# Performance work log

Hardware: AMD Instinct MI355X
Metric: run time of the kernel (lower is better)

## Reference

```python
import jax, jax.numpy as jnp
import numpy as np

DIM_IN, DIM, BS, H, W = 128, 64, 32, 64, 64
G, K = 5, 3          # KAN grid intervals and spline degree
EPS = 1e-5           # BatchNorm eps


def conv2d(x, w, b, groups=1, pad=0):
    # x: [B,C,H,W], w: [O, C//groups, kh, kw]
    y = jax.lax.conv_general_dilated(
        x, w, window_strides=(1, 1), padding=[(pad, pad), (pad, pad)],
        dimension_numbers=('NCHW', 'OIHW', 'NCHW'), feature_group_count=groups)
    return y + b[None, :, None, None]


def bn(x, g, b, m, v):
    # inference-mode BatchNorm2d
    inv = jax.lax.rsqrt(v + EPS)
    return g[None, :, None, None] * (x - m[None, :, None, None]) * inv[None, :, None, None] + b[None, :, None, None]


def make_grid():
    # extended knot vector over [-1,1], G intervals, degree K: G+2K+1 knots
    h = 2.0 / G
    t = jnp.arange(-K, G + K + 1, dtype=jnp.float32) * h - 1.0
    return jnp.broadcast_to(t, (DIM, G + 2 * K + 1))


def bspline_basis(x, t, k):
    # Cox-de Boor recursion. x: [N,in], t: [in, G+2k+1] -> B: [N,in,G+k]
    xe = x[..., None]
    B = ((xe >= t[:, :-1]) & (xe < t[:, 1:])).astype(x.dtype)
    for p in range(1, k + 1):
        B = ((xe - t[:, :-(p + 1)]) / (t[:, p:-1] - t[:, :-(p + 1)])) * B[..., :-1] \
          + ((t[:, p + 1:] - xe) / (t[:, p + 1:] - t[:, 1:-p])) * B[..., 1:]
    return B


def kan_forward(xk, coef, scale_base, scale_sp, kan_bias):
    # single KANLayer [dim -> dim]: silu residual branch + spline branch + node bias
    t = make_grid()
    B = bspline_basis(xk, t, K)                      # [N, in, G+K]
    y_base = jax.nn.silu(xk) @ scale_base            # [N, out]
    y_sp = jnp.einsum('nij,ioj->no', B, coef * scale_sp[:, :, None])
    return y_base + y_sp + kan_bias


def setup_inputs() -> dict:
    key = jax.random.key(0)
    ks = jax.random.split(key, 24)
    rn = lambda k, s, sc=0.05: jax.random.normal(k, s, jnp.float32) * sc
    return {
        'x': jax.random.normal(ks[0], (BS, DIM_IN, H, W), jnp.float32),
        'reduce_w': rn(ks[1], (DIM, DIM_IN, 1, 1), 0.1), 'reduce_b': rn(ks[2], (DIM,)),
        'dw_w': rn(ks[3], (DIM, 1, 7, 7), 0.1), 'dw_b': rn(ks[4], (DIM,)),
        'dw_g': 1.0 + rn(ks[5], (DIM,)), 'dw_beta': rn(ks[6], (DIM,)),
        'dw_m': rn(ks[7], (DIM,)), 'dw_v': 0.5 + jax.random.uniform(ks[8], (DIM,)),
        'f2_w': rn(ks[9], (DIM, DIM, 1, 1), 0.1), 'f2_b': rn(ks[10], (DIM,)),
        'coef': rn(ks[11], (DIM, DIM, G + K), 0.1),
        'scale_base': 1.0 / np.sqrt(DIM) + rn(ks[12], (DIM, DIM)),
        'scale_sp': 1.0 + rn(ks[13], (DIM, DIM)),
        'kan_bias': rn(ks[14], (DIM,)),
        'g_w': rn(ks[15], (DIM, DIM, 1, 1), 0.1), 'g_b': rn(ks[16], (DIM,)),
        'g_g': 1.0 + rn(ks[17], (DIM,)), 'g_beta': rn(ks[18], (DIM,)),
        'g_m': rn(ks[19], (DIM,)), 'g_v': 0.5 + jax.random.uniform(ks[20], (DIM,)),
        'dw2_w': rn(ks[21], (DIM, 1, 7, 7), 0.1), 'dw2_b': rn(ks[22], (DIM,)),
    }


def reference(x, reduce_w, reduce_b, dw_w, dw_b, dw_g, dw_beta, dw_m, dw_v,
              f2_w, f2_b, coef, scale_base, scale_sp, kan_bias,
              g_w, g_b, g_g, g_beta, g_m, g_v, dw2_w, dw2_b):
    x = conv2d(x, reduce_w, reduce_b)                       # dim_reduce 1x1
    inp = x
    xd = bn(conv2d(x, dw_w, dw_b, groups=DIM, pad=3), dw_g, dw_beta, dw_m, dw_v)  # 7x7 dwconv + BN
    bs, dim, h, w = xd.shape
    xk = xd.transpose(0, 2, 3, 1).reshape(bs * h * w, dim)  # tokenwise view
    x1 = kan_forward(xk, coef, scale_base, scale_sp, kan_bias)
    x1 = x1.reshape(bs, h, w, dim).transpose(0, 3, 1, 2)    # back to NCHW
    x2 = conv2d(xd, f2_w, f2_b)                             # f2 1x1
    y = x1 * x2                                             # elementwise gate
    y = bn(conv2d(y, g_w, g_b), g_g, g_beta, g_m, g_v)      # g 1x1 + BN
    y = conv2d(y, dw2_w, dw2_b, groups=DIM, pad=3)          # dwconv2 7x7
    return inp + y
```

## Files before the change

kernel.cpp:

```cpp
#include <hip/hip_runtime.h>
#include <hip/hip_bf16.h>

#define BSZ 32
#define CIN 128
#define CD 64
#define HH 64
#define WW 64
#define PLANE (HH * WW)
#define NPIX (BSZ * HH * WW)
#define NB 8
#define BN_EPS 1e-5f

typedef __attribute__((ext_vector_type(8))) short short8v;
typedef __attribute__((ext_vector_type(4))) float f32x4;
typedef __attribute__((ext_vector_type(4))) unsigned int u32x4;

static __device__ __forceinline__ short f2bf(float f) {
    __hip_bfloat16 h = __float2bfloat16(f);
    return __builtin_bit_cast(short, h);
}
static __device__ __forceinline__ unsigned int cvtpk(float lo, float hi) {
    unsigned int r;
    asm("v_cvt_pk_bf16_f32 %0, %1, %2" : "=v"(r) : "v"(lo), "v"(hi));
    return r;
}

__global__ __launch_bounds__(256) void k_prep(
    const float* __restrict__ coef, const float* __restrict__ ssp,
    const float* __restrict__ sb, const float* __restrict__ f2w,
    const float* __restrict__ reduce_w, const float* __restrict__ g_w,
    const float* __restrict__ dw_g, const float* __restrict__ dw_beta,
    const float* __restrict__ dw_m, const float* __restrict__ dw_v,
    const float* __restrict__ dw_b, const float* __restrict__ g_g,
    const float* __restrict__ g_beta, const float* __restrict__ g_m,
    const float* __restrict__ g_v, const float* __restrict__ g_b,
    short* __restrict__ W1f, short* __restrict__ W2f,
    short* __restrict__ WRf, short* __restrict__ WGf,
    float* __restrict__ cbuf)
{
    const int idx = blockIdx.x * 256 + threadIdx.x;
    if (idx < 36864) {
        const int e = idx & 7, l = (idx >> 3) & 63, c = (idx >> 9) & 3, s = idx >> 11;
        const int k = s * 32 + ((l >> 4) << 3) + e;
        const int j = (c << 4) + (l & 15);
        float v;
        if (k < 512) {
            const int i = k >> 3, t = k & 7;
            v = coef[(i * 64 + j) * 8 + t] * ssp[i * 64 + j];
        } else {
            v = sb[(k - 512) * 64 + j];
        }
        W1f[idx] = f2bf(v);
    } else if (idx < 45056) {
        const int f = idx - 36864;
        const int e = f & 7, l = (f >> 3) & 63, c = (f >> 9) & 3, s = f >> 11;
        const int k = s * 32 + ((l >> 4) << 3) + e;
        const int j = (c << 4) + (l & 15);
        W2f[f] = f2bf(f2w[j * 64 + k]);
    } else if (idx < 53248) {
        const int f = idx - 45056;
        const int e = f & 7, l = (f >> 3) & 63, c = (f >> 9) & 3, s = f >> 11;
        const int k = s * 32 + ((l >> 4) << 3) + e;
        const int j = (c << 4) + (l & 15);
        WRf[f] = f2bf(reduce_w[j * CIN + k]);
    } else if (idx < 57344) {
        const int f = idx - 53248;
        const int e = f & 7, l = (f >> 3) & 63, c = (f >> 9) & 3, s = f >> 11;
        const int k = s * 32 + ((l >> 4) << 3) + e;
        const int j = (c << 4) + (l & 15);
        WGf[f] = f2bf(g_w[j * 64 + k]);
    } else if (idx < 57600) {
        const int q = (idx - 57344) >> 6, c = idx & 63;
        if (q == 0) cbuf[c] = dw_g[c] * rsqrtf(dw_v[c] + BN_EPS);
        else if (q == 1) {
            float sc = dw_g[c] * rsqrtf(dw_v[c] + BN_EPS);
            cbuf[64 + c] = (dw_b[c] - dw_m[c]) * sc + dw_beta[c];
        } else if (q == 2) cbuf[128 + c] = g_g[c] * rsqrtf(g_v[c] + BN_EPS);
// ... 75 lines not shown
    float K[49];
#pragma unroll
    for (int q = 0; q < 49; ++q) K[q] = wp[q];
    const float scl = RESID ? 1.f : sc[c];
    const float shf = shv[c];
    const float* rplane = RESID ? (resid + pbase) : nullptr;
    float* oplane = out + pbase;

    float acc[7] = {0.f, 0.f, 0.f, 0.f, 0.f, 0.f, 0.f};
#pragma unroll
    for (int rr = 0; rr < 22; ++rr) {
        const int ra = H0 + rr - 3;
        float rowv = 0.f;
        if (ra >= 0 && ra < 64) rowv = plane[ra * 64 + lane];
        float sh[7];
        sh[3] = rowv;
#pragma unroll
        for (int d = 1; d <= 3; ++d) {
            float tp = __shfl(rowv, lane + d);
            sh[3 + d] = (lane + d < 64) ? tp : 0.f;
            float tm = __shfl(rowv, lane - d);
            sh[3 - d] = (lane - d >= 0) ? tm : 0.f;
        }
#pragma unroll
        for (int dy = 0; dy < 7; ++dy) {
            const int o = rr - dy;
            if (o >= 0 && o < 16) {
                const int slot = o % 7;
#pragma unroll
                for (int dx = 0; dx < 7; ++dx)
                    acc[slot] = fmaf(sh[dx], K[dy * 7 + dx], acc[slot]);
            }
        }
        const int done = rr - 6;
        if (done >= 0 && done < 16) {
            const int slot = done % 7;
            const int h = H0 + done;
            float val;
            if (RESID) val = acc[slot] + shf + rplane[h * 64 + lane];
            else       val = acc[slot] * scl + shf;
            oplane[h * 64 + lane] = val;
            acc[slot] = 0.f;
        }
    }
}

__global__ __launch_bounds__(256) void k_kan_fused(
    const float* __restrict__ xd, const short* __restrict__ W1f,
    const short* __restrict__ W2f, const short* __restrict__ WGf,
    const float* __restrict__ kb, const float* __restrict__ f2b,
    const float* __restrict__ gs, const float* __restrict__ gsh,
    float* __restrict__ z)
{
    __shared__ __align__(16) short As1[2 * 18 * 64 * 8];
    __shared__ __align__(16) short As2[2 * 2 * 64 * 8];
    const int tid = threadIdx.x;
    const int tg0 = blockIdx.x * 32;
    const int bb = tg0 >> 12, pix0 = tg0 & 4095;
    const float* xb = xd + (size_t)bb * CD * PLANE + pix0;
    const int tkn = tid & 31;
    const int w5 = tid >> 5;
    const int mt = tkn >> 4, m = tkn & 15;

    float vf[8], sf[8];
#pragma unroll
    for (int p = 0; p < 8; ++p) {
        const int c = w5 * 8 + p;
        const float v = xb[(size_t)c * PLANE + tkn];
        vf[p] = v;
        sf[p] = v * __builtin_amdgcn_rcpf(1.0f + __expf(-v));

        const float tt = (v + 2.2f) * 2.5f;
        const float fi = floorf(tt);
        const int i0 = (int)fi;
        const float u = tt - fi;
        const bool inr = (tt >= 0.0f) && (tt < 11.0f);
        const float u2 = u * u, u3 = u2 * u;
        const float t1 = 1.f - u;
        const float w0 = (1.f / 6.f) * t1 * t1 * t1;
        const float w3 = (1.f / 6.f) * u3;
        const float w1 = fmaf(0.5f, u3, 2.f / 3.f) - u2;
        const float w2 = 1.f - w0 - w1 - w3;
        const unsigned W01 = cvtpk(w0, w1);
        const unsigned W23 = cvtpk(w2, w3);
        const int q0 = i0 - 3;
        int a = q0 >> 1;
        const int bpar = q0 & 1;
        if (!inr) a = 100;
        const unsigned A1c = (W01 >> 16) | (W23 << 16);
        const unsigned C0 = bpar ? (W01 << 16) : W01;
        const unsigned C1 = bpar ? A1c : W23;
        const unsigned C2 = bpar ? (W23 >> 16) : 0u;
        u32x4 D;
        D.x = (a == 0) ? C0 : (a == -1) ? C1 : (a == -2) ? C2 : 0u;
        D.y = (a == 1) ? C0 : (a == 0) ? C1 : (a == -1) ? C2 : 0u;
        D.z = (a == 2) ? C0 : (a == 1) ? C1 : (a == 0) ? C2 : 0u;
        D.w = (a == 3) ? C0 : (a == 2) ? C1 : (a == 1) ? C2 : 0u;

        const int s = w5 * 2 + (p >> 2);
        const int phys = (((p & 3) << 4) | m) ^ (s & 7);
        *(u32x4*)&As1[((mt * 18 + s) * 64 + phys) * 8] = D;
    }
    {
        short8v vpk, spk;
#pragma unroll
        for (int q = 0; q < 4; ++q) {
            ((unsigned*)&vpk)[q] = cvtpk(vf[2 * q], vf[2 * q + 1]);
            ((unsigned*)&spk)[q] = cvtpk(sf[2 * q], sf[2 * q + 1]);
        }
        const int slot = ((w5 & 3) << 4) | m;
        const int s2 = 16 + (w5 >> 2);
        *(short8v*)&As1[((mt * 18 + s2) * 64 + (slot ^ (s2 & 7))) * 8] = spk;
        const int s3 = w5 >> 2;
        *(short8v*)&As2[((mt * 2 + s3) * 64 + (slot ^ (s3 & 7))) * 8] = vpk;
    }
    __syncthreads();

    const int cw = tid >> 6, l = tid & 63;
    f32x4 accA0 = {0.f,0.f,0.f,0.f}, accA1 = {0.f,0.f,0.f,0.f};
    f32x4 accB0 = {0.f,0.f,0.f,0.f}, accB1 = {0.f,0.f,0.f,0.f};
#pragma unroll 1
    for (int s = 0; s < 18; ++s) {
        const short8v bfr = *(const short8v*)&W1f[((s * 4 + cw) * 64 + l) * 8];
        const short8v a0 = *(const short8v*)&As1[((0 * 18 + s) * 64 + (l ^ (s & 7))) * 8];
        const short8v a1 = *(const short8v*)&As1[((1 * 18 + s) * 64 + (l ^ (s & 7))) * 8];
        accA0 = __builtin_amdgcn_mfma_f32_16x16x32_bf16(a0, bfr, accA0, 0, 0, 0);
        accA1 = __builtin_amdgcn_mfma_f32_16x16x32_bf16(a1, bfr, accA1, 0, 0, 0);
    }
#pragma unroll
    for (int s = 0; s < 2; ++s) {
        const short8v bfr = *(const short8v*)&W2f[((s * 4 + cw) * 64 + l) * 8];
        const short8v a0 = *(const short8v*)&As2[((0 * 2 + s) * 64 + (l ^ s)) * 8];
        const short8v a1 = *(const short8v*)&As2[((1 * 2 + s) * 64 + (l ^ s)) * 8];
        accB0 = __builtin_amdgcn_mfma_f32_16x16x32_bf16(a0, bfr, accB0, 0, 0, 0);
        accB1 = __builtin_amdgcn_mfma_f32_16x16x32_bf16(a1, bfr, accB1, 0, 0, 0);
    }

    const int j = (cw << 4) + (l & 15);
    const float kbj = kb[j], f2bj = f2b[j];
    const int rb = (l >> 4) << 2;
    float y0[4], y1[4];
#pragma unroll
    for (int r = 0; r < 4; ++r) {
        y0[r] = (accA0[r] + kbj) * (accB0[r] + f2bj);
        y1[r] = (accA1[r] + kbj) * (accB1[r] + f2bj);
    }
    __syncthreads();

    float* Ysh = (float*)As1;
#pragma unroll
    for (int r = 0; r < 4; ++r) {
        Ysh[j * 33 + rb + r]      = y0[r];
        Ysh[j * 33 + 16 + rb + r] = y1[r];
    }
    __syncthreads();

    {
        float yv[8];
#pragma unroll
        for (int p = 0; p < 8; ++p) yv[p] = Ysh[(w5 * 8 + p) * 33 + tkn];
        short8v ypk;
#pragma unroll
        for (int q = 0; q < 4; ++q)
            ((unsigned*)&ypk)[q] = cvtpk(yv[2 * q], yv[2 * q + 1]);
        const int slot = ((w5 & 3) << 4) | m;
        const int s3 = w5 >> 2;
        *(short8v*)&As2[((mt * 2 + s3) * 64 + (slot ^ (s3 & 7))) * 8] = ypk;
    }
    __syncthreads();

    f32x4 acc30 = {0.f,0.f,0.f,0.f}, acc31 = {0.f,0.f,0.f,0.f};
#pragma unroll
    for (int s = 0; s < 2; ++s) {
        const short8v bfr = *(const short8v*)&WGf[((s * 4 + cw) * 64 + l) * 8];
        const short8v a0 = *(const short8v*)&As2[((0 * 2 + s) * 64 + (l ^ s)) * 8];
        const short8v a1 = *(const short8v*)&As2[((1 * 2 + s) * 64 + (l ^ s)) * 8];
        acc30 = __builtin_amdgcn_mfma_f32_16x16x32_bf16(a0, bfr, acc30, 0, 0, 0);
        acc31 = __builtin_amdgcn_mfma_f32_16x16x32_bf16(a1, bfr, acc31, 0, 0, 0);
    }

    float* Osh = (float*)As1;
    const float sj = gs[j], hj = gsh[j];
#pragma unroll
    for (int r = 0; r < 4; ++r) {
        Osh[j * 33 + rb + r]      = acc30[r] * sj + hj;
        Osh[j * 33 + 16 + rb + r] = acc31[r] * sj + hj;
    }
    __syncthreads();
    float* zb = z + (size_t)bb * CD * PLANE + pix0;
#pragma unroll
    for (int q = 0; q < 8; ++q) {
        const int idx = tid + (q << 8);
        const int jj = idx >> 5, t2 = idx & 31;
        zb[(size_t)jj * PLANE + t2] = Osh[jj * 33 + t2];
    }
}

extern "C" void kernel_launch(void* const* d_in, const int* in_sizes, int n_in,
                              void* d_out, int out_size, void* d_ws, size_t ws_size,
                              hipStream_t stream)
{
    (void)in_sizes; (void)n_in; (void)out_size; (void)ws_size;
    const float* x        = (const float*)d_in[0];
    const float* reduce_w = (const float*)d_in[1];
    const float* reduce_b = (const float*)d_in[2];
    const float* dw_w     = (const float*)d_in[3];
    const float* dw_b     = (const float*)d_in[4];
    const float* dw_g     = (const float*)d_in[5];
    const float* dw_beta  = (const float*)d_in[6];
    const float* dw_m     = (const float*)d_in[7];
    const float* dw_v     = (const float*)d_in[8];
    const float* f2_w     = (const float*)d_in[9];
    const float* f2_b     = (const float*)d_in[10];
    const float* coef     = (const float*)d_in[11];
    const float* sbase    = (const float*)d_in[12];
    const float* ssp      = (const float*)d_in[13];
    const float* kbias    = (const float*)d_in[14];
    const float* g_w      = (const float*)d_in[15];
    const float* g_b      = (const float*)d_in[16];
    const float* g_g      = (const float*)d_in[17];
    const float* g_beta   = (const float*)d_in[18];
    const float* g_m      = (const float*)d_in[19];
    const float* g_v      = (const float*)d_in[20];
    const float* dw2_w    = (const float*)d_in[21];
    const float* dw2_b    = (const float*)d_in[22];
    float* out = (float*)d_out;

    const size_t NEL = (size_t)BSZ * CD * PLANE;
    short* W1f = (short*)d_ws;
    short* W2f = W1f + 36864;
    short* WRf = W2f + 8192;
    short* WGf = WRf + 8192;
    float* cbuf = (float*)((char*)d_ws + 115200);
    float* inp = (float*)((char*)d_ws + 131072);
    float* xdb = inp + NEL;
    float* z   = xdb + NEL;

    k_prep<<<225, 256, 0, stream>>>(coef, ssp, sbase, f2_w, reduce_w, g_w,
                                    dw_g, dw_beta, dw_m, dw_v, dw_b,
                                    g_g, g_beta, g_m, g_v, g_b,
                                    W1f, W2f, WRf, WGf, cbuf);
    k_reduce_mfma<<<BSZ * 32, 256, 0, stream>>>(x, WRf, reduce_b, inp);
    k_dwconv<false><<<BSZ * 16 * 4, 256, 0, stream>>>(inp, dw_w, cbuf, cbuf + 64, nullptr, xdb);
    k_kan_fused<<<NPIX / 32, 256, 0, stream>>>(xdb, W1f, W2f, WGf, kbias, f2_b,
                                               cbuf + 128, cbuf + 192, z);
    k_dwconv<true><<<BSZ * 16 * 4, 256, 0, stream>>>(z, dw2_w, nullptr, dw2_b, inp, out);
}
```

Baseline: 105.8 us.

## Process KAN fused tile as two 16-token passes to halve LDS use

The fused KAN/gate/g-conv kernel previously staged all 32 tokens per block in shared memory at once and kept two MFMA accumulator sets per wave. It now loops over two 16-token halves, reusing a half-size LDS buffer and a single accumulator set, with each thread computing 4 channels instead of 8. This cuts LDS footprint and register pressure to allow higher occupancy. The cost is extra barriers per block, weight fragments reloaded from global memory for each half, and 16-wide global stores that coalesce worse.

```diff
diff --git a/kernel.cpp b/kernel.cpp
--- a/kernel.cpp
+++ b/kernel.cpp
@@ -204,147 +204,135 @@
     const float* __restrict__ gs, const float* __restrict__ gsh,
     float* __restrict__ z)
 {
-    __shared__ __align__(16) short As1[2 * 18 * 64 * 8];
-    __shared__ __align__(16) short As2[2 * 2 * 64 * 8];
+    __shared__ __align__(16) short As1[18 * 64 * 8];
+    __shared__ __align__(16) short As2[2 * 64 * 8];
     const int tid = threadIdx.x;
     const int tg0 = blockIdx.x * 32;
     const int bb = tg0 >> 12, pix0 = tg0 & 4095;
     const float* xb = xd + (size_t)bb * CD * PLANE + pix0;
-    const int tkn = tid & 31;
-    const int w5 = tid >> 5;
-    const int mt = tkn >> 4, m = tkn & 15;
-
-    float vf[8], sf[8];
-#pragma unroll
-    for (int p = 0; p < 8; ++p) {
-        const int c = w5 * 8 + p;
-        const float v = xb[(size_t)c * PLANE + tkn];
-        vf[p] = v;
-        sf[p] = v * __builtin_amdgcn_rcpf(1.0f + __expf(-v));
-
-        const float tt = (v + 2.2f) * 2.5f;
-        const float fi = floorf(tt);
-        const int i0 = (int)fi;
-        const float u = tt - fi;
-        const bool inr = (tt >= 0.0f) && (tt < 11.0f);
-        const float u2 = u * u, u3 = u2 * u;
-        const float t1 = 1.f - u;
-        const float w0 = (1.f / 6.f) * t1 * t1 * t1;
-        const float w3 = (1.f / 6.f) * u3;
-        const float w1 = fmaf(0.5f, u3, 2.f / 3.f) - u2;
-        const float w2 = 1.f - w0 - w1 - w3;
-        const unsigned W01 = cvtpk(w0, w1);
-        const unsigned W23 = cvtpk(w2, w3);
-        const int q0 = i0 - 3;
-        int a = q0 >> 1;
-        const int bpar = q0 & 1;
-        if (!inr) a = 100;
-        const unsigned A1c = (W01 >> 16) | (W23 << 16);
-        const unsigned C0 = bpar ? (W01 << 16) : W01;
-        const unsigned C1 = bpar ? A1c : W23;
-        const unsigned C2 = bpar ? (W23 >> 16) : 0u;
-        u32x4 D;
-        D.x = (a == 0) ? C0 : (a == -1) ? C1 : (a == -2) ? C2 : 0u;
-        D.y = (a == 1) ? C0 : (a == 0) ? C1 : (a == -1) ? C2 : 0u;
-        D.z = (a == 2) ? C0 : (a == 1) ? C1 : (a == 0) ? C2 : 0u;
-        D.w = (a == 3) ? C0 : (a == 2) ? C1 : (a == 1) ? C2 : 0u;
-
-        const int s = w5 * 2 + (p >> 2);
-        const int phys = (((p & 3) << 4) | m) ^ (s & 7);
-        *(u32x4*)&As1[((mt * 18 + s) * 64 + phys) * 8] = D;
-    }
-    {
-        short8v vpk, spk;
+    float* zb = z + (size_t)bb * CD * PLANE + pix0;
+    const int tkn = tid & 15;
+    const int grp = tid >> 4;
+    const int m = tkn;
+    const int cw = tid >> 6, l = tid & 63;
+    const int j = (cw << 4) + (l & 15);
+    const int rb = (l >> 4) << 2;
+    const float kbj = kb[j], f2bj = f2b[j];
+    const float sj = gs[j], hj = gsh[j];
+    const int gfield = (grp >> 1) & 3;
+    const int slot16 = (gfield << 4) | m;
+    const int e0 = (grp & 1) * 4;
+
+#pragma unroll 1
+    for (int g = 0; g < 2; ++g) {
+        const int toff = g * 16;
+        float vf[4], sf[4];
+#pragma unroll
+        for (int p = 0; p < 4; ++p) {
+            const int c = grp * 4 + p;
+            const float v = xb[(size_t)c * PLANE + toff + tkn];
+            vf[p] = v;
+            sf[p] = v * __builtin_amdgcn_rcpf(1.0f + __expf(-v));
+
+            const float tt = (v + 2.2f) * 2.5f;
+            const float fi = floorf(tt);
+            const int i0 = (int)fi;
+            const float u = tt - fi;
+            const bool inr = (tt >= 0.0f) && (tt < 11.0f);
+            const float u2 = u * u, u3 = u2 * u;
+            const float t1 = 1.f - u;
+            const float w0 = (1.f / 6.f) * t1 * t1 * t1;
+            const float w3 = (1.f / 6.f) * u3;
+            const float w1 = fmaf(0.5f, u3, 2.f / 3.f) - u2;
+            const float w2 = 1.f - w0 - w1 - w3;
+            const unsigned W01 = cvtpk(w0, w1);
+            const unsigned W23 = cvtpk(w2, w3);
+            const int q0 = i0 - 3;
+            int a = q0 >> 1;
+            const int bpar = q0 & 1;
+            if (!inr) a = 100;
+            const unsigned A1c = (W01 >> 16) | (W23 << 16);
+            const unsigned C0 = bpar ? (W01 << 16) : W01;
+            const unsigned C1 = bpar ? A1c : W23;
+            const unsigned C2 = bpar ? (W23 >> 16) : 0u;
+            u32x4 D;
+            D.x = (a == 0) ? C0 : (a == -1) ? C1 : (a == -2) ? C2 : 0u;
+            D.y = (a == 1) ? C0 : (a == 0) ? C1 : (a == -1) ? C2 : 0u;
+            D.z = (a == 2) ? C0 : (a == 1) ? C1 : (a == 0) ? C2 : 0u;
+            D.w = (a == 3) ? C0 : (a == 2) ? C1 : (a == 1) ? C2 : 0u;
+
+            const int s = c >> 2;
+            const int phys = ((p << 4) | m) ^ (s & 7);
+            *(u32x4*)&As1[(s * 64 + phys) * 8] = D;
+        }
+        {
+            uint2 sv, vv;
+            sv.x = cvtpk(sf[0], sf[1]); sv.y = cvtpk(sf[2], sf[3]);
+            vv.x = cvtpk(vf[0], vf[1]); vv.y = cvtpk(vf[2], vf[3]);
+            const int s2 = 16 + (grp >> 3);
+            *(uint2*)&As1[(s2 * 64 + (slot16 ^ (s2 & 7))) * 8 + e0] = sv;
+            const int s3 = grp >> 3;
+            *(uint2*)&As2[(s3 * 64 + (slot16 ^ (s3 & 7))) * 8 + e0] = vv;
+        }
+        __syncthreads();
+
+        f32x4 accA = {0.f,0.f,0.f,0.f}, accB = {0.f,0.f,0.f,0.f};
+#pragma unroll 1
+        for (int s = 0; s < 18; ++s) {
+            const short8v bfr = *(const short8v*)&W1f[((s * 4 + cw) * 64 + l) * 8];
+            const short8v a0 = *(const short8v*)&As1[(s * 64 + (l ^ (s & 7))) * 8];
+            accA = __builtin_amdgcn_mfma_f32_16x16x32_bf16(a0, bfr, accA, 0, 0, 0);
+        }
+#pragma unroll
+        for (int s = 0; s < 2; ++s) {
+            const short8v bfr = *(const short8v*)&W2f[((s * 4 + cw) * 64 + l) * 8];
+            const short8v a0 = *(const short8v*)&As2[(s * 64 + (l ^ s)) * 8];
+            accB = __builtin_amdgcn_mfma_f32_16x16x32_bf16(a0, bfr, accB, 0, 0, 0);
+        }
+
+        float y0[4];
+#pragma unroll
+        for (int r = 0; r < 4; ++r)
+            y0[r] = (accA[r] + kbj) * (accB[r] + f2bj);
+        __syncthreads();
+
+        float* Ysh = (float*)As1;
+#pragma unroll
+        for (int r = 0; r < 4; ++r) Ysh[j * 17 + rb + r] = y0[r];
+        __syncthreads();
+
+        {
+            float yv[4];
+#pragma unroll
+            for (int p = 0; p < 4; ++p) yv[p] = Ysh[(grp * 4 + p) * 17 + tkn];
+            uint2 yy;
+            yy.x = cvtpk(yv[0], yv[1]); yy.y = cvtpk(yv[2], yv[3]);
+            const int s3 = grp >> 3;
+            *(uint2*)&As2[(s3 * 64 + (slot16 ^ (s3 & 7))) * 8 + e0] = yy;
+        }
+        __syncthreads();
+
+        f32x4 acc3 = {0.f,0.f,0.f,0.f};
+#pragma unroll
+        for (int s = 0; s < 2; ++s) {
+            const short8v bfr = *(const short8v*)&WGf[((s * 4 + cw) * 64 + l) * 8];
+            const short8v a0 = *(const short8v*)&As2[(s * 64 + (l ^ s)) * 8];
+            acc3 = __builtin_amdgcn_mfma_f32_16x16x32_bf16(a0, bfr, acc3, 0, 0, 0);
+        }
+
+        float* Osh = (float*)As1;
+#pragma unroll
+        for (int r = 0; r < 4; ++r)
+            Osh[j * 17 + rb + r] = acc3[r] * sj + hj;
+        __syncthreads();
+
 #pragma unroll
         for (int q = 0; q < 4; ++q) {
-            ((unsigned*)&vpk)[q] = cvtpk(vf[2 * q], vf[2 * q + 1]);
-            ((unsigned*)&spk)[q] = cvtpk(sf[2 * q], sf[2 * q + 1]);
-        }
-        const int slot = ((w5 & 3) << 4) | m;
-        const int s2 = 16 + (w5 >> 2);
-        *(short8v*)&As1[((mt * 18 + s2) * 64 + (slot ^ (s2 & 7))) * 8] = spk;
-        const int s3 = w5 >> 2;
-        *(short8v*)&As2[((mt * 2 + s3) * 64 + (slot ^ (s3 & 7))) * 8] = vpk;
-    }
-    __syncthreads();
-
-    const int cw = tid >> 6, l = tid & 63;
-    f32x4 accA0 = {0.f,0.f,0.f,0.f}, accA1 = {0.f,0.f,0.f,0.f};
-    f32x4 accB0 = {0.f,0.f,0.f,0.f}, accB1 = {0.f,0.f,0.f,0.f};
-#pragma unroll 1
-    for (int s = 0; s < 18; ++s) {
-        const short8v bfr = *(const short8v*)&W1f[((s * 4 + cw) * 64 + l) * 8];
-        const short8v a0 = *(const short8v*)&As1[((0 * 18 + s) * 64 + (l ^ (s & 7))) * 8];
-        const short8v a1 = *(const short8v*)&As1[((1 * 18 + s) * 64 + (l ^ (s & 7))) * 8];
-        accA0 = __builtin_amdgcn_mfma_f32_16x16x32_bf16(a0, bfr, accA0, 0, 0, 0);
-        accA1 = __builtin_amdgcn_mfma_f32_16x16x32_bf16(a1, bfr, accA1, 0, 0, 0);
-    }
-#pragma unroll
-    for (int s = 0; s < 2; ++s) {
-        const short8v bfr = *(const short8v*)&W2f[((s * 4 + cw) * 64 + l) * 8];
-        const short8v a0 = *(const short8v*)&As2[((0 * 2 + s) * 64 + (l ^ s)) * 8];
-        const short8v a1 = *(const short8v*)&As2[((1 * 2 + s) * 64 + (l ^ s)) * 8];
-        accB0 = __builtin_amdgcn_mfma_f32_16x16x32_bf16(a0, bfr, accB0, 0, 0, 0);
-        accB1 = __builtin_amdgcn_mfma_f32_16x16x32_bf16(a1, bfr, accB1, 0, 0, 0);
-    }
-
-    const int j = (cw << 4) + (l & 15);
-    const float kbj = kb[j], f2bj = f2b[j];
-    const int rb = (l >> 4) << 2;
-    float y0[4], y1[4];
-#pragma unroll
-    for (int r = 0; r < 4; ++r) {
-        y0[r] = (accA0[r] + kbj) * (accB0[r] + f2bj);
-        y1[r] = (accA1[r] + kbj) * (accB1[r] + f2bj);
-    }
-    __syncthreads();
-
-    float* Ysh = (float*)As1;
-#pragma unroll
-    for (int r = 0; r < 4; ++r) {
-        Ysh[j * 33 + rb + r]      = y0[r];
-        Ysh[j * 33 + 16 + rb + r] = y1[r];
-    }
-    __syncthreads();
-
-    {
-        float yv[8];
-#pragma unroll
-        for (int p = 0; p < 8; ++p) yv[p] = Ysh[(w5 * 8 + p) * 33 + tkn];
-        short8v ypk;
-#pragma unroll
-        for (int q = 0; q < 4; ++q)
-            ((unsigned*)&ypk)[q] = cvtpk(yv[2 * q], yv[2 * q + 1]);
-        const int slot = ((w5 & 3) << 4) | m;
-        const int s3 = w5 >> 2;
-        *(short8v*)&As2[((mt * 2 + s3) * 64 + (slot ^ (s3 & 7))) * 8] = ypk;
-    }
-    __syncthreads();
-
-    f32x4 acc30 = {0.f,0.f,0.f,0.f}, acc31 = {0.f,0.f,0.f,0.f};
-#pragma unroll
-    for (int s = 0; s < 2; ++s) {
-        const short8v bfr = *(const short8v*)&WGf[((s * 4 + cw) * 64 + l) * 8];
-        const short8v a0 = *(const short8v*)&As2[((0 * 2 + s) * 64 + (l ^ s)) * 8];
-        const short8v a1 = *(const short8v*)&As2[((1 * 2 + s) * 64 + (l ^ s)) * 8];
-        acc30 = __builtin_amdgcn_mfma_f32_16x16x32_bf16(a0, bfr, acc30, 0, 0, 0);
-        acc31 = __builtin_amdgcn_mfma_f32_16x16x32_bf16(a1, bfr, acc31, 0, 0, 0);
-    }
-
-    float* Osh = (float*)As1;
-    const float sj = gs[j], hj = gsh[j];
-#pragma unroll
-    for (int r = 0; r < 4; ++r) {
-        Osh[j * 33 + rb + r]      = acc30[r] * sj + hj;
-        Osh[j * 33 + 16 + rb + r] = acc31[r] * sj + hj;
-    }
-    __syncthreads();
-    float* zb = z + (size_t)bb * CD * PLANE + pix0;
-#pragma unroll
-    for (int q = 0; q < 8; ++q) {
-        const int idx = tid + (q << 8);
-        const int jj = idx >> 5, t2 = idx & 31;
-        zb[(size_t)jj * PLANE + t2] = Osh[jj * 33 + t2];
+            const int idx = tid + (q << 8);
+            const int jj = idx >> 4, t2 = idx & 15;
+            zb[(size_t)jj * PLANE + toff + t2] = Osh[jj * 17 + t2];
+        }
+        __syncthreads();
     }
 }
 
```

Measured after the change: 112.6 us. 6.4% more time.

## Process two token tiles per KAN block with register-resident weights and prefetch

Applied to the files above, without the earlier changes.

The fused KAN/gate kernel now handles 64 tokens per block in two 32-token iterations, half the blocks. The bf16 weight fragments (W1, W2, WG) are loaded into registers once per block instead of once per tile. The next tile's input is prefetched into registers while the current one is processed. This raises register pressure (about 88 VGPRs of weights), which may lower occupancy, and the tile loop adds one extra barrier per iteration.

```diff
diff --git a/kernel.cpp b/kernel.cpp
--- a/kernel.cpp
+++ b/kernel.cpp
@@ -207,144 +207,166 @@
     __shared__ __align__(16) short As1[2 * 18 * 64 * 8];
     __shared__ __align__(16) short As2[2 * 2 * 64 * 8];
     const int tid = threadIdx.x;
-    const int tg0 = blockIdx.x * 32;
+    const int tg0 = blockIdx.x * 64;
     const int bb = tg0 >> 12, pix0 = tg0 & 4095;
     const float* xb = xd + (size_t)bb * CD * PLANE + pix0;
+    float* zb = z + (size_t)bb * CD * PLANE + pix0;
     const int tkn = tid & 31;
     const int w5 = tid >> 5;
     const int mt = tkn >> 4, m = tkn & 15;
-
-    float vf[8], sf[8];
-#pragma unroll
-    for (int p = 0; p < 8; ++p) {
-        const int c = w5 * 8 + p;
-        const float v = xb[(size_t)c * PLANE + tkn];
-        vf[p] = v;
-        sf[p] = v * __builtin_amdgcn_rcpf(1.0f + __expf(-v));
-
-        const float tt = (v + 2.2f) * 2.5f;
-        const float fi = floorf(tt);
-        const int i0 = (int)fi;
-        const float u = tt - fi;
-        const bool inr = (tt >= 0.0f) && (tt < 11.0f);
-        const float u2 = u * u, u3 = u2 * u;
-        const float t1 = 1.f - u;
-        const float w0 = (1.f / 6.f) * t1 * t1 * t1;
-        const float w3 = (1.f / 6.f) * u3;
-        const float w1 = fmaf(0.5f, u3, 2.f / 3.f) - u2;
-        const float w2 = 1.f - w0 - w1 - w3;
-        const unsigned W01 = cvtpk(w0, w1);
-        const unsigned W23 = cvtpk(w2, w3);
-        const int q0 = i0 - 3;
-        int a = q0 >> 1;
-        const int bpar = q0 & 1;
-        if (!inr) a = 100;
-        const unsigned A1c = (W01 >> 16) | (W23 << 16);
-        const unsigned C0 = bpar ? (W01 << 16) : W01;
-        const unsigned C1 = bpar ? A1c : W23;
-        const unsigned C2 = bpar ? (W23 >> 16) : 0u;
-        u32x4 D;
-        D.x = (a == 0) ? C0 : (a == -1) ? C1 : (a == -2) ? C2 : 0u;
-        D.y = (a == 1) ? C0 : (a == 0) ? C1 : (a == -1) ? C2 : 0u;
-        D.z = (a == 2) ? C0 : (a == 1) ? C1 : (a == 0) ? C2 : 0u;
-        D.w = (a == 3) ? C0 : (a == 2) ? C1 : (a == 1) ? C2 : 0u;
-
-        const int s = w5 * 2 + (p >> 2);
-        const int phys = (((p & 3) << 4) | m) ^ (s & 7);
-        *(u32x4*)&As1[((mt * 18 + s) * 64 + phys) * 8] = D;
-    }
-    {
-        short8v vpk, spk;
-#pragma unroll
-        for (int q = 0; q < 4; ++q) {
-            ((unsigned*)&vpk)[q] = cvtpk(vf[2 * q], vf[2 * q + 1]);
-            ((unsigned*)&spk)[q] = cvtpk(sf[2 * q], sf[2 * q + 1]);
-        }
-        const int slot = ((w5 & 3) << 4) | m;
-        const int s2 = 16 + (w5 >> 2);
-        *(short8v*)&As1[((mt * 18 + s2) * 64 + (slot ^ (s2 & 7))) * 8] = spk;
-        const int s3 = w5 >> 2;
-        *(short8v*)&As2[((mt * 2 + s3) * 64 + (slot ^ (s3 & 7))) * 8] = vpk;
-    }
-    __syncthreads();
-
     const int cw = tid >> 6, l = tid & 63;
-    f32x4 accA0 = {0.f,0.f,0.f,0.f}, accA1 = {0.f,0.f,0.f,0.f};
-    f32x4 accB0 = {0.f,0.f,0.f,0.f}, accB1 = {0.f,0.f,0.f,0.f};
+    const int j = (cw << 4) + (l & 15);
+    const int rb = (l >> 4) << 2;
+    const float kbj = kb[j], f2bj = f2b[j];
+    const float sj = gs[j], hj = gsh[j];
+
+    short8v w1r[18];
+#pragma unroll
+    for (int s = 0; s < 18; ++s)
+        w1r[s] = *(const short8v*)&W1f[((s * 4 + cw) * 64 + l) * 8];
+    short8v w2r[2], wgr[2];
+#pragma unroll
+    for (int s = 0; s < 2; ++s) {
+        w2r[s] = *(const short8v*)&W2f[((s * 4 + cw) * 64 + l) * 8];
+        wgr[s] = *(const short8v*)&WGf[((s * 4 + cw) * 64 + l) * 8];
+    }
+
+    float vcur[8];
+#pragma unroll
+    for (int p = 0; p < 8; ++p)
+        vcur[p] = xb[(size_t)(w5 * 8 + p) * PLANE + tkn];
+
 #pragma unroll 1
-    for (int s = 0; s < 18; ++s) {
-        const short8v bfr = *(const short8v*)&W1f[((s * 4 + cw) * 64 + l) * 8];
-        const short8v a0 = *(const short8v*)&As1[((0 * 18 + s) * 64 + (l ^ (s & 7))) * 8];
-        const short8v a1 = *(const short8v*)&As1[((1 * 18 + s) * 64 + (l ^ (s & 7))) * 8];
-        accA0 = __builtin_amdgcn_mfma_f32_16x16x32_bf16(a0, bfr, accA0, 0, 0, 0);
-        accA1 = __builtin_amdgcn_mfma_f32_16x16x32_bf16(a1, bfr, accA1, 0, 0, 0);
-    }
-#pragma unroll
-    for (int s = 0; s < 2; ++s) {
-        const short8v bfr = *(const short8v*)&W2f[((s * 4 + cw) * 64 + l) * 8];
-        const short8v a0 = *(const short8v*)&As2[((0 * 2 + s) * 64 + (l ^ s)) * 8];
-        const short8v a1 = *(const short8v*)&As2[((1 * 2 + s) * 64 + (l ^ s)) * 8];
-        accB0 = __builtin_amdgcn_mfma_f32_16x16x32_bf16(a0, bfr, accB0, 0, 0, 0);
-        accB1 = __builtin_amdgcn_mfma_f32_16x16x32_bf16(a1, bfr, accB1, 0, 0, 0);
-    }
-
-    const int j = (cw << 4) + (l & 15);
-    const float kbj = kb[j], f2bj = f2b[j];
-    const int rb = (l >> 4) << 2;
-    float y0[4], y1[4];
-#pragma unroll
-    for (int r = 0; r < 4; ++r) {
-        y0[r] = (accA0[r] + kbj) * (accB0[r] + f2bj);
-        y1[r] = (accA1[r] + kbj) * (accB1[r] + f2bj);
-    }
-    __syncthreads();
-
-    float* Ysh = (float*)As1;
-#pragma unroll
-    for (int r = 0; r < 4; ++r) {
-        Ysh[j * 33 + rb + r]      = y0[r];
-        Ysh[j * 33 + 16 + rb + r] = y1[r];
-    }
-    __syncthreads();
-
-    {
-        float yv[8];
-#pragma unroll
-        for (int p = 0; p < 8; ++p) yv[p] = Ysh[(w5 * 8 + p) * 33 + tkn];
-        short8v ypk;
-#pragma unroll
-        for (int q = 0; q < 4; ++q)
-            ((unsigned*)&ypk)[q] = cvtpk(yv[2 * q], yv[2 * q + 1]);
-        const int slot = ((w5 & 3) << 4) | m;
-        const int s3 = w5 >> 2;
-        *(short8v*)&As2[((mt * 2 + s3) * 64 + (slot ^ (s3 & 7))) * 8] = ypk;
-    }
-    __syncthreads();
-
-    f32x4 acc30 = {0.f,0.f,0.f,0.f}, acc31 = {0.f,0.f,0.f,0.f};
-#pragma unroll
-    for (int s = 0; s < 2; ++s) {
-        const short8v bfr = *(const short8v*)&WGf[((s * 4 + cw) * 64 + l) * 8];
-        const short8v a0 = *(const short8v*)&As2[((0 * 2 + s) * 64 + (l ^ s)) * 8];
-        const short8v a1 = *(const short8v*)&As2[((1 * 2 + s) * 64 + (l ^ s)) * 8];
-        acc30 = __builtin_amdgcn_mfma_f32_16x16x32_bf16(a0, bfr, acc30, 0, 0, 0);
-        acc31 = __builtin_amdgcn_mfma_f32_16x16x32_bf16(a1, bfr, acc31, 0, 0, 0);
-    }
-
-    float* Osh = (float*)As1;
-    const float sj = gs[j], hj = gsh[j];
-#pragma unroll
-    for (int r = 0; r < 4; ++r) {
-        Osh[j * 33 + rb + r]      = acc30[r] * sj + hj;
-        Osh[j * 33 + 16 + rb + r] = acc31[r] * sj + hj;
-    }
-    __syncthreads();
-    float* zb = z + (size_t)bb * CD * PLANE + pix0;
-#pragma unroll
-    for (int q = 0; q < 8; ++q) {
-        const int idx = tid + (q << 8);
-        const int jj = idx >> 5, t2 = idx & 31;
-        zb[(size_t)jj * PLANE + t2] = Osh[jj * 33 + t2];
+    for (int t = 0; t < 2; ++t) {
+        const int toff = t * 32;
+        float vf[8], sf[8];
+#pragma unroll
+        for (int p = 0; p < 8; ++p) {
+            const float v = vcur[p];
+            vf[p] = v;
+            sf[p] = v * __builtin_amdgcn_rcpf(1.0f + __expf(-v));
+
+            const float tt = (v + 2.2f) * 2.5f;
+            const float fi = floorf(tt);
+            const int i0 = (int)fi;
+            const float u = tt - fi;
+            const bool inr = (tt >= 0.0f) && (tt < 11.0f);
+            const float u2 = u * u, u3 = u2 * u;
+            const float t1 = 1.f - u;
+            const float w0 = (1.f / 6.f) * t1 * t1 * t1;
+            const float w3 = (1.f / 6.f) * u3;
+            const float w1 = fmaf(0.5f, u3, 2.f / 3.f) - u2;
+            const float w2 = 1.f - w0 - w1 - w3;
+            const unsigned W01 = cvtpk(w0, w1);
+            const unsigned W23 = cvtpk(w2, w3);
+            const int q0 = i0 - 3;
+            int a = q0 >> 1;
+            const int bpar = q0 & 1;
+            if (!inr) a = 100;
+            const unsigned A1c = (W01 >> 16) | (W23 << 16);
+            const unsigned C0 = bpar ? (W01 << 16) : W01;
+            const unsigned C1 = bpar ? A1c : W23;
+            const unsigned C2 = bpar ? (W23 >> 16) : 0u;
+            u32x4 D;
+            D.x = (a == 0) ? C0 : (a == -1) ? C1 : (a == -2) ? C2 : 0u;
+            D.y = (a == 1) ? C0 : (a == 0) ? C1 : (a == -1) ? C2 : 0u;
+            D.z = (a == 2) ? C0 : (a == 1) ? C1 : (a == 0) ? C2 : 0u;
+            D.w = (a == 3) ? C0 : (a == 2) ? C1 : (a == 1) ? C2 : 0u;
+
+            const int s = w5 * 2 + (p >> 2);
+            const int phys = (((p & 3) << 4) | m) ^ (s & 7);
+            *(u32x4*)&As1[((mt * 18 + s) * 64 + phys) * 8] = D;
+        }
+        {
+            short8v vpk, spk;
+#pragma unroll
+            for (int q = 0; q < 4; ++q) {
+                ((unsigned*)&vpk)[q] = cvtpk(vf[2 * q], vf[2 * q + 1]);
+                ((unsigned*)&spk)[q] = cvtpk(sf[2 * q], sf[2 * q + 1]);
+            }
+            const int slot = ((w5 & 3) << 4) | m;
+            const int s2 = 16 + (w5 >> 2);
+            *(short8v*)&As1[((mt * 18 + s2) * 64 + (slot ^ (s2 & 7))) * 8] = spk;
+            const int s3 = w5 >> 2;
+            *(short8v*)&As2[((mt * 2 + s3) * 64 + (slot ^ (s3 & 7))) * 8] = vpk;
+        }
+        if (t == 0) {
+#pragma unroll
+            for (int p = 0; p < 8; ++p)
+                vcur[p] = xb[(size_t)(w5 * 8 + p) * PLANE + 32 + tkn];
+        }
+        __syncthreads();
+
+        f32x4 accA0 = {0.f,0.f,0.f,0.f}, accA1 = {0.f,0.f,0.f,0.f};
+        f32x4 accB0 = {0.f,0.f,0.f,0.f}, accB1 = {0.f,0.f,0.f,0.f};
+#pragma unroll
+        for (int s = 0; s < 18; ++s) {
+            const short8v a0 = *(const short8v*)&As1[((0 * 18 + s) * 64 + (l ^ (s & 7))) * 8];
+            const short8v a1 = *(const short8v*)&As1[((1 * 18 + s) * 64 + (l ^ (s & 7))) * 8];
+            accA0 = __builtin_amdgcn_mfma_f32_16x16x32_bf16(a0, w1r[s], accA0, 0, 0, 0);
+            accA1 = __builtin_amdgcn_mfma_f32_16x16x32_bf16(a1, w1r[s], accA1, 0, 0, 0);
+        }
+#pragma unroll
+        for (int s = 0; s < 2; ++s) {
+            const short8v a0 = *(const short8v*)&As2[((0 * 2 + s) * 64 + (l ^ s)) * 8];
+            const short8v a1 = *(const short8v*)&As2[((1 * 2 + s) * 64 + (l ^ s)) * 8];
+            accB0 = __builtin_amdgcn_mfma_f32_16x16x32_bf16(a0, w2r[s], accB0, 0, 0, 0);
+            accB1 = __builtin_amdgcn_mfma_f32_16x16x32_bf16(a1, w2r[s], accB1, 0, 0, 0);
+        }
+
+        float y0[4], y1[4];
+#pragma unroll
+        for (int r = 0; r < 4; ++r) {
+            y0[r] = (accA0[r] + kbj) * (accB0[r] + f2bj);
+            y1[r] = (accA1[r] + kbj) * (accB1[r] + f2bj);
+        }
+        __syncthreads();
+
+        float* Ysh = (float*)As1;
+#pragma unroll
+        for (int r = 0; r < 4; ++r) {
+            Ysh[j * 33 + rb + r]      = y0[r];
+            Ysh[j * 33 + 16 + rb + r] = y1[r];
+        }
+        __syncthreads();
+
+        {
+            float yv[8];
+#pragma unroll
+            for (int p = 0; p < 8; ++p) yv[p] = Ysh[(w5 * 8 + p) * 33 + tkn];
+            short8v ypk;
+#pragma unroll
+            for (int q = 0; q < 4; ++q)
+                ((unsigned*)&ypk)[q] = cvtpk(yv[2 * q], yv[2 * q + 1]);
+            const int slot = ((w5 & 3) << 4) | m;
+            const int s3 = w5 >> 2;
+            *(short8v*)&As2[((mt * 2 + s3) * 64 + (slot ^ (s3 & 7))) * 8] = ypk;
+        }
+        __syncthreads();
+
+        f32x4 acc30 = {0.f,0.f,0.f,0.f}, acc31 = {0.f,0.f,0.f,0.f};
+#pragma unroll
+        for (int s = 0; s < 2; ++s) {
+            const short8v a0 = *(const short8v*)&As2[((0 * 2 + s) * 64 + (l ^ s)) * 8];
+            const short8v a1 = *(const short8v*)&As2[((1 * 2 + s) * 64 + (l ^ s)) * 8];
+            acc30 = __builtin_amdgcn_mfma_f32_16x16x32_bf16(a0, wgr[s], acc30, 0, 0, 0);
+            acc31 = __builtin_amdgcn_mfma_f32_16x16x32_bf16(a1, wgr[s], acc31, 0, 0, 0);
+        }
+
+        float* Osh = (float*)As1;
+#pragma unroll
+        for (int r = 0; r < 4; ++r) {
+            Osh[j * 33 + rb + r]      = acc30[r] * sj + hj;
+            Osh[j * 33 + 16 + rb + r] = acc31[r] * sj + hj;
+        }
+        __syncthreads();
+#pragma unroll
+        for (int q = 0; q < 8; ++q) {
+            const int idx = tid + (q << 8);
+            const int jj = idx >> 5, t2 = idx & 31;
+            zb[(size_t)jj * PLANE + toff + t2] = Osh[jj * 33 + t2];
+        }
+        __syncthreads();
     }
 }
 
@@ -394,7 +416,7 @@
                                     W1f, W2f, WRf, WGf, cbuf);
     k_reduce_mfma<<<BSZ * 32, 256, 0, stream>>>(x, WRf, reduce_b, inp);
     k_dwconv<false><<<BSZ * 16 * 4, 256, 0, stream>>>(inp, dw_w, cbuf, cbuf + 64, nullptr, xdb);
-    k_kan_fused<<<NPIX / 32, 256, 0, stream>>>(xdb, W1f, W2f, WGf, kbias, f2_b,
+    k_kan_fused<<<NPIX / 64, 256, 0, stream>>>(xdb, W1f, W2f, WGf, kbias, f2_b,
                                                cbuf + 128, cbuf + 192, z);
     k_dwconv<true><<<BSZ * 16 * 4, 256, 0, stream>>>(z, dw2_w, nullptr, dw2_b, inp, out);
 }
```

After: 105.0 us. No clear change (-0.8%).

## Restructure KAN kernel so each wave owns 32 tokens across all output channels

Applied to the files above, without the earlier changes.

The fused KAN kernel now gives each wavefront its own 32 tokens and computes all 64 output channels per wave, instead of splitting the output channels across waves that share tokens. B-spline basis fragments are built in registers straight into MFMA operands. Only small per-wave LDS scratch is used for the silu, identity and gate transposes, so every block-wide barrier is removed. Blocks cover 128 tokens, which adds more accumulator registers per thread and may lower occupancy. Weight fragments are now reread from global or cache by every wave.

```diff
diff --git a/kernel.cpp b/kernel.cpp
--- a/kernel.cpp
+++ b/kernel.cpp
@@ -23,6 +23,35 @@
     unsigned int r;
     asm("v_cvt_pk_bf16_f32 %0, %1, %2" : "=v"(r) : "v"(lo), "v"(hi));
     return r;
+}
+static __device__ __forceinline__ u32x4 basisD(float v) {
+    const float tt = (v + 2.2f) * 2.5f;
+    const float fi = floorf(tt);
+    const int i0 = (int)fi;
+    const float u = tt - fi;
+    const bool inr = (tt >= 0.0f) && (tt < 11.0f);
+    const float u2 = u * u, u3 = u2 * u;
+    const float t1 = 1.f - u;
+    const float w0 = (1.f / 6.f) * t1 * t1 * t1;
+    const float w3 = (1.f / 6.f) * u3;
+    const float w1 = fmaf(0.5f, u3, 2.f / 3.f) - u2;
+    const float w2 = 1.f - w0 - w1 - w3;
+    const unsigned W01 = cvtpk(w0, w1);
+    const unsigned W23 = cvtpk(w2, w3);
+    const int q0 = i0 - 3;
+    int a = q0 >> 1;
+    const int bpar = q0 & 1;
+    if (!inr) a = 100;
+    const unsigned A1c = (W01 >> 16) | (W23 << 16);
+    const unsigned C0 = bpar ? (W01 << 16) : W01;
+    const unsigned C1 = bpar ? A1c : W23;
+    const unsigned C2 = bpar ? (W23 >> 16) : 0u;
+    u32x4 D;
+    D.x = (a == 0) ? C0 : (a == -1) ? C1 : (a == -2) ? C2 : 0u;
+    D.y = (a == 1) ? C0 : (a == 0) ? C1 : (a == -1) ? C2 : 0u;
+    D.z = (a == 2) ? C0 : (a == 1) ? C1 : (a == 0) ? C2 : 0u;
+    D.w = (a == 3) ? C0 : (a == 2) ? C1 : (a == 1) ? C2 : 0u;
+    return D;
 }
 
 __global__ __launch_bounds__(256) void k_prep(
@@ -204,147 +233,150 @@
     const float* __restrict__ gs, const float* __restrict__ gsh,
     float* __restrict__ z)
 {
-    __shared__ __align__(16) short As1[2 * 18 * 64 * 8];
-    __shared__ __align__(16) short As2[2 * 2 * 64 * 8];
+    __shared__ unsigned svS[4][1088];
+    __shared__ unsigned svV[4][1088];
     const int tid = threadIdx.x;
-    const int tg0 = blockIdx.x * 32;
+    const int wv = tid >> 6, l = tid & 63;
+    const int hi = l >> 4, m = l & 15;
+    const int tg0 = blockIdx.x * 128 + wv * 32;
     const int bb = tg0 >> 12, pix0 = tg0 & 4095;
     const float* xb = xd + (size_t)bb * CD * PLANE + pix0;
-    const int tkn = tid & 31;
-    const int w5 = tid >> 5;
-    const int mt = tkn >> 4, m = tkn & 15;
-
-    float vf[8], sf[8];
-#pragma unroll
-    for (int p = 0; p < 8; ++p) {
-        const int c = w5 * 8 + p;
-        const float v = xb[(size_t)c * PLANE + tkn];
-        vf[p] = v;
-        sf[p] = v * __builtin_amdgcn_rcpf(1.0f + __expf(-v));
-
-        const float tt = (v + 2.2f) * 2.5f;
-        const float fi = floorf(tt);
-        const int i0 = (int)fi;
-        const float u = tt - fi;
-        const bool inr = (tt >= 0.0f) && (tt < 11.0f);
-        const float u2 = u * u, u3 = u2 * u;
-        const float t1 = 1.f - u;
-        const float w0 = (1.f / 6.f) * t1 * t1 * t1;
-        const float w3 = (1.f / 6.f) * u3;
-        const float w1 = fmaf(0.5f, u3, 2.f / 3.f) - u2;
-        const float w2 = 1.f - w0 - w1 - w3;
-        const unsigned W01 = cvtpk(w0, w1);
-        const unsigned W23 = cvtpk(w2, w3);
-        const int q0 = i0 - 3;
-        int a = q0 >> 1;
-        const int bpar = q0 & 1;
-        if (!inr) a = 100;
-        const unsigned A1c = (W01 >> 16) | (W23 << 16);
-        const unsigned C0 = bpar ? (W01 << 16) : W01;
-        const unsigned C1 = bpar ? A1c : W23;
-        const unsigned C2 = bpar ? (W23 >> 16) : 0u;
-        u32x4 D;
-        D.x = (a == 0) ? C0 : (a == -1) ? C1 : (a == -2) ? C2 : 0u;
-        D.y = (a == 1) ? C0 : (a == 0) ? C1 : (a == -1) ? C2 : 0u;
-        D.z = (a == 2) ? C0 : (a == 1) ? C1 : (a == 0) ? C2 : 0u;
-        D.w = (a == 3) ? C0 : (a == 2) ? C1 : (a == 1) ? C2 : 0u;
-
-        const int s = w5 * 2 + (p >> 2);
-        const int phys = (((p & 3) << 4) | m) ^ (s & 7);
-        *(u32x4*)&As1[((mt * 18 + s) * 64 + phys) * 8] = D;
-    }
-    {
-        short8v vpk, spk;
-#pragma unroll
-        for (int q = 0; q < 4; ++q) {
-            ((unsigned*)&vpk)[q] = cvtpk(vf[2 * q], vf[2 * q + 1]);
-            ((unsigned*)&spk)[q] = cvtpk(sf[2 * q], sf[2 * q + 1]);
-        }
-        const int slot = ((w5 & 3) << 4) | m;
-        const int s2 = 16 + (w5 >> 2);
-        *(short8v*)&As1[((mt * 18 + s2) * 64 + (slot ^ (s2 & 7))) * 8] = spk;
-        const int s3 = w5 >> 2;
-        *(short8v*)&As2[((mt * 2 + s3) * 64 + (slot ^ (s3 & 7))) * 8] = vpk;
-    }
-    __syncthreads();
-
-    const int cw = tid >> 6, l = tid & 63;
-    f32x4 accA0 = {0.f,0.f,0.f,0.f}, accA1 = {0.f,0.f,0.f,0.f};
-    f32x4 accB0 = {0.f,0.f,0.f,0.f}, accB1 = {0.f,0.f,0.f,0.f};
-#pragma unroll 1
-    for (int s = 0; s < 18; ++s) {
-        const short8v bfr = *(const short8v*)&W1f[((s * 4 + cw) * 64 + l) * 8];
-        const short8v a0 = *(const short8v*)&As1[((0 * 18 + s) * 64 + (l ^ (s & 7))) * 8];
-        const short8v a1 = *(const short8v*)&As1[((1 * 18 + s) * 64 + (l ^ (s & 7))) * 8];
-        accA0 = __builtin_amdgcn_mfma_f32_16x16x32_bf16(a0, bfr, accA0, 0, 0, 0);
-        accA1 = __builtin_amdgcn_mfma_f32_16x16x32_bf16(a1, bfr, accA1, 0, 0, 0);
-    }
-#pragma unroll
-    for (int s = 0; s < 2; ++s) {
-        const short8v bfr = *(const short8v*)&W2f[((s * 4 + cw) * 64 + l) * 8];
-        const short8v a0 = *(const short8v*)&As2[((0 * 2 + s) * 64 + (l ^ s)) * 8];
-        const short8v a1 = *(const short8v*)&As2[((1 * 2 + s) * 64 + (l ^ s)) * 8];
-        accB0 = __builtin_amdgcn_mfma_f32_16x16x32_bf16(a0, bfr, accB0, 0, 0, 0);
-        accB1 = __builtin_amdgcn_mfma_f32_16x16x32_bf16(a1, bfr, accB1, 0, 0, 0);
-    }
-
-    const int j = (cw << 4) + (l & 15);
-    const float kbj = kb[j], f2bj = f2b[j];
-    const int rb = (l >> 4) << 2;
-    float y0[4], y1[4];
-#pragma unroll
-    for (int r = 0; r < 4; ++r) {
-        y0[r] = (accA0[r] + kbj) * (accB0[r] + f2bj);
-        y1[r] = (accA1[r] + kbj) * (accB1[r] + f2bj);
-    }
-    __syncthreads();
-
-    float* Ysh = (float*)As1;
-#pragma unroll
-    for (int r = 0; r < 4; ++r) {
-        Ysh[j * 33 + rb + r]      = y0[r];
-        Ysh[j * 33 + 16 + rb + r] = y1[r];
-    }
-    __syncthreads();
-
-    {
-        float yv[8];
-#pragma unroll
-        for (int p = 0; p < 8; ++p) yv[p] = Ysh[(w5 * 8 + p) * 33 + tkn];
-        short8v ypk;
-#pragma unroll
-        for (int q = 0; q < 4; ++q)
-            ((unsigned*)&ypk)[q] = cvtpk(yv[2 * q], yv[2 * q + 1]);
-        const int slot = ((w5 & 3) << 4) | m;
-        const int s3 = w5 >> 2;
-        *(short8v*)&As2[((mt * 2 + s3) * 64 + (slot ^ (s3 & 7))) * 8] = ypk;
-    }
-    __syncthreads();
-
-    f32x4 acc30 = {0.f,0.f,0.f,0.f}, acc31 = {0.f,0.f,0.f,0.f};
-#pragma unroll
-    for (int s = 0; s < 2; ++s) {
-        const short8v bfr = *(const short8v*)&WGf[((s * 4 + cw) * 64 + l) * 8];
-        const short8v a0 = *(const short8v*)&As2[((0 * 2 + s) * 64 + (l ^ s)) * 8];
-        const short8v a1 = *(const short8v*)&As2[((1 * 2 + s) * 64 + (l ^ s)) * 8];
-        acc30 = __builtin_amdgcn_mfma_f32_16x16x32_bf16(a0, bfr, acc30, 0, 0, 0);
-        acc31 = __builtin_amdgcn_mfma_f32_16x16x32_bf16(a1, bfr, acc31, 0, 0, 0);
-    }
-
-    float* Osh = (float*)As1;
-    const float sj = gs[j], hj = gsh[j];
-#pragma unroll
-    for (int r = 0; r < 4; ++r) {
-        Osh[j * 33 + rb + r]      = acc30[r] * sj + hj;
-        Osh[j * 33 + 16 + rb + r] = acc31[r] * sj + hj;
-    }
-    __syncthreads();
     float* zb = z + (size_t)bb * CD * PLANE + pix0;
-#pragma unroll
-    for (int q = 0; q < 8; ++q) {
-        const int idx = tid + (q << 8);
-        const int jj = idx >> 5, t2 = idx & 31;
-        zb[(size_t)jj * PLANE + t2] = Osh[jj * 33 + t2];
+    unsigned* sS = svS[wv];
+    unsigned* sV = svV[wv];
+
+    float kbj[4], f2bj[4], sj[4], hj[4];
+#pragma unroll
+    for (int jt = 0; jt < 4; ++jt) {
+        const int j = jt * 16 + m;
+        kbj[jt] = kb[j]; f2bj[jt] = f2b[j]; sj[jt] = gs[j]; hj[jt] = gsh[j];
+    }
+
+    float xv0[16], xv1[16];
+#pragma unroll
+    for (int s = 0; s < 16; ++s) {
+        xv0[s] = xb[(size_t)(4 * s + hi) * PLANE + m];
+        xv1[s] = xb[(size_t)(4 * s + hi) * PLANE + 16 + m];
+    }
+
+    f32x4 accA0[4], accA1[4];
+#pragma unroll
+    for (int jt = 0; jt < 4; ++jt) {
+        accA0[jt] = (f32x4){0.f, 0.f, 0.f, 0.f};
+        accA1[jt] = (f32x4){0.f, 0.f, 0.f, 0.f};
+    }
+
+#pragma unroll
+    for (int s = 0; s < 16; ++s) {
+        const int c = 4 * s + hi;
+        const float v0 = xv0[s], v1 = xv1[s];
+        const float sl0 = v0 * __builtin_amdgcn_rcpf(1.0f + __expf(-v0));
+        const float sl1 = v1 * __builtin_amdgcn_rcpf(1.0f + __expf(-v1));
+        sS[c * 17 + m] = cvtpk(sl0, sl1);
+        sV[c * 17 + m] = cvtpk(v0, v1);
+        const short8v a0 = __builtin_bit_cast(short8v, basisD(v0));
+        const short8v a1 = __builtin_bit_cast(short8v, basisD(v1));
+#pragma unroll
+        for (int jt = 0; jt < 4; ++jt) {
+            const short8v bfr = *(const short8v*)&W1f[((s * 4 + jt) * 64 + l) * 8];
+            accA0[jt] = __builtin_amdgcn_mfma_f32_16x16x32_bf16(a0, bfr, accA0[jt], 0, 0, 0);
+            accA1[jt] = __builtin_amdgcn_mfma_f32_16x16x32_bf16(a1, bfr, accA1[jt], 0, 0, 0);
+        }
+    }
+
+#pragma unroll
+    for (int s2 = 0; s2 < 2; ++s2) {
+        unsigned q[8];
+#pragma unroll
+        for (int e = 0; e < 8; ++e)
+            q[e] = sS[(s2 * 32 + 8 * hi + e) * 17 + m];
+        short8v f0, f1;
+#pragma unroll
+        for (int qi = 0; qi < 4; ++qi) {
+            ((unsigned*)&f0)[qi] = (q[2 * qi] & 0xffffu) | (q[2 * qi + 1] << 16);
+            ((unsigned*)&f1)[qi] = (q[2 * qi] >> 16) | (q[2 * qi + 1] & 0xffff0000u);
+        }
+#pragma unroll
+        for (int jt = 0; jt < 4; ++jt) {
+            const short8v bfr = *(const short8v*)&W1f[(((16 + s2) * 4 + jt) * 64 + l) * 8];
+            accA0[jt] = __builtin_amdgcn_mfma_f32_16x16x32_bf16(f0, bfr, accA0[jt], 0, 0, 0);
+            accA1[jt] = __builtin_amdgcn_mfma_f32_16x16x32_bf16(f1, bfr, accA1[jt], 0, 0, 0);
+        }
+    }
+
+    f32x4 accB0[4], accB1[4];
+#pragma unroll
+    for (int jt = 0; jt < 4; ++jt) {
+        accB0[jt] = (f32x4){0.f, 0.f, 0.f, 0.f};
+        accB1[jt] = (f32x4){0.f, 0.f, 0.f, 0.f};
+    }
+#pragma unroll
+    for (int s3 = 0; s3 < 2; ++s3) {
+        unsigned q[8];
+#pragma unroll
+        for (int e = 0; e < 8; ++e)
+            q[e] = sV[(s3 * 32 + 8 * hi + e) * 17 + m];
+        short8v f0, f1;
+#pragma unroll
+        for (int qi = 0; qi < 4; ++qi) {
+            ((unsigned*)&f0)[qi] = (q[2 * qi] & 0xffffu) | (q[2 * qi + 1] << 16);
+            ((unsigned*)&f1)[qi] = (q[2 * qi] >> 16) | (q[2 * qi + 1] & 0xffff0000u);
+        }
+#pragma unroll
+        for (int jt = 0; jt < 4; ++jt) {
+            const short8v bfr = *(const short8v*)&W2f[((s3 * 4 + jt) * 64 + l) * 8];
+            accB0[jt] = __builtin_amdgcn_mfma_f32_16x16x32_bf16(f0, bfr, accB0[jt], 0, 0, 0);
+            accB1[jt] = __builtin_amdgcn_mfma_f32_16x16x32_bf16(f1, bfr, accB1[jt], 0, 0, 0);
+        }
+    }
+
+    const int rb = hi * 4;
+#pragma unroll
+    for (int jt = 0; jt < 4; ++jt)
+#pragma unroll
+        for (int r = 0; r < 4; ++r) {
+            const float ya = (accA0[jt][r] + kbj[jt]) * (accB0[jt][r] + f2bj[jt]);
+            const float yb2 = (accA1[jt][r] + kbj[jt]) * (accB1[jt][r] + f2bj[jt]);
+            sS[(jt * 16 + m) * 17 + rb + r] = cvtpk(ya, yb2);
+        }
+
+    f32x4 acc30[4], acc31[4];
+#pragma unroll
+    for (int jt = 0; jt < 4; ++jt) {
+        acc30[jt] = (f32x4){0.f, 0.f, 0.f, 0.f};
+        acc31[jt] = (f32x4){0.f, 0.f, 0.f, 0.f};
+    }
+#pragma unroll
+    for (int s3 = 0; s3 < 2; ++s3) {
+        unsigned q[8];
+#pragma unroll
+        for (int e = 0; e < 8; ++e)
+            q[e] = sS[(s3 * 32 + 8 * hi + e) * 17 + m];
+        short8v f0, f1;
+#pragma unroll
+        for (int qi = 0; qi < 4; ++qi) {
+            ((unsigned*)&f0)[qi] = (q[2 * qi] & 0xffffu) | (q[2 * qi + 1] << 16);
+            ((unsigned*)&f1)[qi] = (q[2 * qi] >> 16) | (q[2 * qi + 1] & 0xffff0000u);
+        }
+#pragma unroll
+        for (int jt = 0; jt < 4; ++jt) {
+            const short8v bfr = *(const short8v*)&WGf[((s3 * 4 + jt) * 64 + l) * 8];
+            acc30[jt] = __builtin_amdgcn_mfma_f32_16x16x32_bf16(f0, bfr, acc30[jt], 0, 0, 0);
+            acc31[jt] = __builtin_amdgcn_mfma_f32_16x16x32_bf16(f1, bfr, acc31[jt], 0, 0, 0);
+        }
+    }
+
+#pragma unroll
+    for (int jt = 0; jt < 4; ++jt) {
+        const int j = jt * 16 + m;
+        f32x4 o0, o1;
+#pragma unroll
+        for (int r = 0; r < 4; ++r) {
+            o0[r] = acc30[jt][r] * sj[jt] + hj[jt];
+            o1[r] = acc31[jt][r] * sj[jt] + hj[jt];
+        }
+        *(f32x4*)&zb[(size_t)j * PLANE + rb] = o0;
+        *(f32x4*)&zb[(size_t)j * PLANE + 16 + rb] = o1;
     }
 }
 
@@ -394,7 +426,7 @@
                                     W1f, W2f, WRf, WGf, cbuf);
     k_reduce_mfma<<<BSZ * 32, 256, 0, stream>>>(x, WRf, reduce_b, inp);
     k_dwconv<false><<<BSZ * 16 * 4, 256, 0, stream>>>(inp, dw_w, cbuf, cbuf + 64, nullptr, xdb);
-    k_kan_fused<<<NPIX / 32, 256, 0, stream>>>(xdb, W1f, W2f, WGf, kbias, f2_b,
-                                               cbuf + 128, cbuf + 192, z);
+    k_kan_fused<<<NPIX / 128, 256, 0, stream>>>(xdb, W1f, W2f, WGf, kbias, f2_b,
+                                                cbuf + 128, cbuf + 192, z);
     k_dwconv<true><<<BSZ * 16 * 4, 256, 0, stream>>>(z, dw2_w, nullptr, dw2_b, inp, out);
 }
```

Result: faster. 100.1 us (-5.4%).
